# Optimization experiments

Measured on AMD Instinct MI355X. Metric: run time of the kernel, lower is better.

Reference implementation:

```python
import jax, jax.numpy as jnp
import numpy as np

NEG_INF = float('-inf')


def setup_inputs() -> dict:
    key = jax.random.key(0)
    k1, k2, k3, k4 = jax.random.split(key, 4)
    B, S, D, C = 32, 1024, 1024, 64
    emb_sentences = jax.random.normal(k1, (B, S, D), dtype=jnp.float32)
    att_sentences = jax.random.bernoulli(k2, 0.5, (B, S))
    W = jax.random.normal(k3, (D, C), dtype=jnp.float32) * (1.0 / np.sqrt(D))
    b = jax.random.normal(k4, (C,), dtype=jnp.float32) * 0.01
    return {"emb_sentences": emb_sentences, "att_sentences": att_sentences, "W": W, "b": b}


def reference(emb_sentences, att_sentences, W, b):
    # Original: gather valid tokens -> Linear classifier -> scatter into
    # a -inf-filled [B, S, C] logits tensor. Dense-equivalent (jit-friendly):
    # compute logits everywhere and mask invalid positions to -inf; masked
    # tokens never flow through the MLP in the original, and jnp.where
    # reproduces exactly that (values and gradients).
    dense = jnp.einsum('bsd,dc->bsc', emb_sentences, W) + b  # [B,S,C]
    logits = jnp.where(att_sentences[:, :, None], dense, NEG_INF)
    # get_labels: argmax, then -1 wherever the row was -inf-filled
    labels = jnp.argmax(logits, axis=-1)
    labels = jnp.where(logits[:, :, 0] == NEG_INF, -1, labels)
    return labels, logits
```

## Files before the change

kernel.cpp:

```cpp
#include <hip/hip_runtime.h>
#include <hip/hip_bf16.h>
#include <hip/hip_fp16.h>
#include <math.h>
#include <float.h>

#define ROWS 32768
#define DDIM 1024
#define CDIM 64

#define MASKED_LOGIT_BITS 0xFF7F0000u

typedef __attribute__((ext_vector_type(8))) _Float16 f16x8;
typedef __attribute__((ext_vector_type(4))) float f32x4;

#define BFRAG_BYTES (32 * 2 * 4 * 64 * 16)

__device__ __forceinline__ void split8(float4 a, float4 b, f16x8& h, f16x8& l) {
    float f[8] = {a.x, a.y, a.z, a.w, b.x, b.y, b.z, b.w};
#pragma unroll
    for (int j = 0; j < 8; ++j) {
        _Float16 t = (_Float16)f[j];
        h[j] = t;
        l[j] = (_Float16)(f[j] - (float)t);
    }
}

__global__ __launch_bounds__(256) void bprep_kernel(const float* __restrict__ W,
                                                    unsigned char* __restrict__ bf) {
    const int ks = blockIdx.x;
    const int t  = threadIdx.x;
    const int g  = t >> 6, c = t & 63;
    float vv[8];
#pragma unroll
    for (int j = 0; j < 8; ++j)
        vv[j] = W[(size_t)(ks * 32 + g * 8 + j) * CDIM + c];
    f16x8 hi, lo;
    split8(make_float4(vv[0], vv[1], vv[2], vv[3]),
           make_float4(vv[4], vv[5], vv[6], vv[7]), hi, lo);
    const int nt = c >> 4;
    const int lane = g * 16 + (c & 15);
    *(f16x8*)(bf + ((size_t)((ks * 2 + 0) * 4 + nt) * 64 + lane) * 16) = hi;
    *(f16x8*)(bf + ((size_t)((ks * 2 + 1) * 4 + nt) * 64 + lane) * 16) = lo;
}

#define MBR 64
#define NRND 8
#define KSR 128

__global__ __launch_bounds__(512, 4) void dense_mfma_kernel(
    const float* __restrict__ emb, const int* __restrict__ att,
    const unsigned char* __restrict__ bf, const float* __restrict__ bias,
    float* __restrict__ out) {
    __shared__ f16x8 Af[4][2][4][64];
    __shared__ f16x8 Bl[4][2][4][64];
    __shared__ float pv[4][16][2], pc[4][16][2];

    const int start = blockIdx.x * MBR;
    const int tid = threadIdx.x;
    const int lane = tid & 63;
    const int wv = tid >> 6;
    const int mr = wv & 3, np = wv >> 2;

    const int srow = tid & 63;
    const int kseg = (tid >> 6) * 16;
    const bool sval = (att[start + srow] != 0);
    const float* __restrict__ sp = emb + (size_t)(start + srow) * DDIM + kseg;
    const int ssub = kseg >> 5;
    const int sg0  = (kseg & 31) >> 3;
    const int smr  = srow >> 4;
    const int sl0  = sg0 * 16 + (srow & 15);
    const int sl1  = sl0 + 16;

    const f16x8* __restrict__ bsrc0 = (const f16x8*)bf + (size_t)tid * 4;
    f16x8* const bdst = (f16x8*)Bl + (size_t)tid * 4;

    f32x4 hh0 = {0,0,0,0}, ml0 = {0,0,0,0}, hh1 = {0,0,0,0}, ml1 = {0,0,0,0};

    float4 x0 = {0,0,0,0}, x1 = {0,0,0,0}, x2 = {0,0,0,0}, x3 = {0,0,0,0};
    if (sval) {
        x0 = *(const float4*)(sp);
        x1 = *(const float4*)(sp + 4);
        x2 = *(const float4*)(sp + 8);
        x3 = *(const float4*)(sp + 12);
    }
    f16x8 y0 = bsrc0[0], y1 = bsrc0[1], y2 = bsrc0[2], y3 = bsrc0[3];

    const int nt0 = np * 2, nt1 = np * 2 + 1;

#pragma unroll 1
    for (int t = 0; t < NRND; ++t) {
        __syncthreads();
        {
            f16x8 h0, l0, h1, l1;
            split8(x0, x1, h0, l0);
            split8(x2, x3, h1, l1);
            Af[ssub][0][smr][sl0] = h0;
            Af[ssub][1][smr][sl0] = l0;
            Af[ssub][0][smr][sl1] = h1;
            Af[ssub][1][smr][sl1] = l1;
            bdst[0] = y0; bdst[1] = y1; bdst[2] = y2; bdst[3] = y3;
        }
        __syncthreads();

        const bool more = (t + 1 < NRND);
        if (more) {
            if (sval) {
                const float* q = sp + (t + 1) * KSR;
                x0 = *(const float4*)(q);
                x1 = *(const float4*)(q + 4);
                x2 = *(const float4*)(q + 8);
                x3 = *(const float4*)(q + 12);
            }
            const f16x8* bs = bsrc0 + (size_t)(t + 1) * 2048;
            y0 = bs[0]; y1 = bs[1]; y2 = bs[2]; y3 = bs[3];
        }

#pragma unroll
        for (int s = 0; s < 4; ++s) {
            f16x8 ah = Af[s][0][mr][lane];
            f16x8 al = Af[s][1][mr][lane];
            f16x8 bh0 = Bl[s][0][nt0][lane];
            f16x8 bl0 = Bl[s][1][nt0][lane];
            f16x8 bh1 = Bl[s][0][nt1][lane];
            f16x8 bl1 = Bl[s][1][nt1][lane];
            hh0 = __builtin_amdgcn_mfma_f32_16x16x32_f16(ah, bh0, hh0, 0, 0, 0);
            ml0 = __builtin_amdgcn_mfma_f32_16x16x32_f16(al, bh0, ml0, 0, 0, 0);
            ml0 = __builtin_amdgcn_mfma_f32_16x16x32_f16(ah, bl0, ml0, 0, 0, 0);
            hh1 = __builtin_amdgcn_mfma_f32_16x16x32_f16(ah, bh1, hh1, 0, 0, 0);
            ml1 = __builtin_amdgcn_mfma_f32_16x16x32_f16(al, bh1, ml1, 0, 0, 0);
            ml1 = __builtin_amdgcn_mfma_f32_16x16x32_f16(ah, bl1, ml1, 0, 0, 0);
        }
    }

    f32x4 c0 = hh0 + ml0;
    f32x4 c1 = hh1 + ml1;
    const int n0 = np * 32 + (lane & 15);
    const float bz0 = bias[n0], bz1 = bias[n0 + 16];
    const float sent = __uint_as_float(MASKED_LOGIT_BITS);
    float* labels = out;
    float* logits = out + ROWS;

#pragma unroll
    for (int q = 0; q < 4; ++q) {
        int rl = mr * 16 + (lane >> 4) * 4 + q;
        int grow = start + rl;
        bool v = (att[grow] != 0);
        float v0 = v ? (c0[q] + bz0) : sent;
        float v1 = v ? (c1[q] + bz1) : sent;
        logits[(size_t)grow * CDIM + n0]      = v0;
        logits[(size_t)grow * CDIM + n0 + 16] = v1;
        float bv; float bc;
        if (v1 > v0) { bv = v1; bc = (float)(n0 + 16); }
        else         { bv = v0; bc = (float)n0; }
#pragma unroll
        for (int m = 1; m < 16; m <<= 1) {
            float ov = __shfl_xor(bv, m);
            float oc = __shfl_xor(bc, m);
            if (ov > bv || (ov == bv && oc < bc)) { bv = ov; bc = oc; }
        }
        if ((lane & 15) == 0) { pv[mr][rl & 15][np] = bv; pc[mr][rl & 15][np] = bc; }
    }
    __syncthreads();

    if (tid < MBR) {
        int grow = start + tid;
        if (att[grow] != 0) {
            int m = tid >> 4, r = tid & 15;
            labels[grow] = (pv[m][r][1] > pv[m][r][0]) ? pc[m][r][1] : pc[m][r][0];
        } else {
            labels[grow] = -1.0f;
        }
    }
}

#define BR 16
#define KT 64
#define NQ 4
#define NRv 4
#define QSPAN (NRv * KT)

__global__ void zero_counter_kernel(int* __restrict__ cnt) {
    if (threadIdx.x == 0) *cnt = 0;
}

__global__ __launch_bounds__(256) void compact_kernel(const int* __restrict__ att,
                                                      float* __restrict__ out,
                                                      int* __restrict__ cnt,
                                                      int* __restrict__ list) {
    int row = blockIdx.x * 256 + threadIdx.x;
    int lane = threadIdx.x & 63;
    bool valid = (att[row] != 0);
    unsigned long long ball = __ballot(valid);
    int total = __popcll(ball);
    int base = 0;
    if (lane == 0 && total > 0) base = atomicAdd(cnt, total);
    base = __shfl(base, 0);
    if (valid) {
        int prefix = __popcll(ball & ((1ull << lane) - 1ull));
        list[base + prefix] = row;
    } else {
        out[row] = -1.0f;
    }
}

__global__ __launch_bounds__(256) void fill_kernel(const int* __restrict__ att,
                                                   float* __restrict__ out) {
    int gid = blockIdx.x * 256 + threadIdx.x;
    int row = gid >> 4;
    int q   = gid & 15;
    if (att[row] != 0) return;
    float s = __uint_as_float(MASKED_LOGIT_BITS);
    float4 sv = make_float4(s, s, s, s);
    float* logits = out + ROWS;
    *(float4*)(logits + (size_t)row * CDIM + q * 4) = sv;
}

__global__ __launch_bounds__(512, 8) void row_gemm_kernel(const float* __restrict__ emb,
                                                          const float* __restrict__ W,
                                                          const float* __restrict__ bias,
                                                          const int* __restrict__ cnt,
                                                          const int* __restrict__ list,
                                                          float* __restrict__ out) {
    __shared__ float smem[2 * NQ * BR * KT];
    const int nValid = *cnt;
    const int start = blockIdx.x * BR;
    if (start >= nValid) return;
    const int tid  = threadIdx.x;
    const int lane = tid & 63;
    const int wv   = tid >> 6;
    const int q    = wv >> 1;
    const int rg   = (wv & 1) * 8;
    const int srow = tid >> 5;
    const int sq   = (tid >> 3) & 3;
    const int soff = (tid & 7) * 4;
    int sidx = start + srow;
    int sr = list[(sidx < nValid) ? sidx : start];
    const float* __restrict__ sp = emb + (size_t)sr * DDIM + sq * QSPAN + soff;
    float* const sdst0 = &smem[((0 * NQ + sq) * BR + srow) * KT + soff];
    float* const sdst1 = &smem[((1 * NQ + sq) * BR + srow) * KT + soff];
    float acc[8];
#pragma unroll
    for (int r = 0; r < 8; ++r) acc[r] = 0.0f;
    {
        float4 a0 = *(const float4*)(sp);
        float4 a1 = *(const float4*)(sp + 32);
        *(float4*)(sdst0)      = a0;
        *(float4*)(sdst0 + 32) = a1;
    }
    __syncthreads();
    const float* const ebase0 = &smem[((0 * NQ + q) * BR + rg) * KT];
    const float* const ebase1 = &smem[((1 * NQ + q) * BR + rg) * KT];
#pragma unroll 1
    for (int t = 0; t < NRv; ++t) {
        float4 n0, n1;
        const bool more = (t + 1 < NRv);
        if (more) {
            const float* qq = sp + (t + 1) * KT;
            n0 = *(const float4*)(qq);
            n1 = *(const float4*)(qq + 32);
        }
        const float* __restrict__ wp = W + (size_t)(q * QSPAN + t * KT) * CDIM + lane;
        const float* __restrict__ eb = (t & 1) ? ebase1 : ebase0;
#pragma unroll 2
        for (int c8 = 0; c8 < KT; c8 += 8) {
            float w0 = wp[0 * CDIM]; float w1 = wp[1 * CDIM];
            float w2 = wp[2 * CDIM]; float w3 = wp[3 * CDIM];
            float w4 = wp[4 * CDIM]; float w5 = wp[5 * CDIM];
            float w6 = wp[6 * CDIM]; float w7 = wp[7 * CDIM];
            wp += 8 * CDIM;
            const float* ep0 = eb + c8;
#pragma unroll
            for (int r = 0; r < 8; ++r) {
                const float* ep = ep0 + r * KT;
                float4 ea = *(const float4*)(ep);
                float4 ev = *(const float4*)(ep + 4);
                acc[r] = fmaf(ea.x, w0, acc[r]); acc[r] = fmaf(ea.y, w1, acc[r]);
                acc[r] = fmaf(ea.z, w2, acc[r]); acc[r] = fmaf(ea.w, w3, acc[r]);
                acc[r] = fmaf(ev.x, w4, acc[r]); acc[r] = fmaf(ev.y, w5, acc[r]);
                acc[r] = fmaf(ev.z, w6, acc[r]); acc[r] = fmaf(ev.w, w7, acc[r]);
            }
        }
        if (more) {
            float* d = (t & 1) ? sdst0 : sdst1;
            *(float4*)(d)      = n0;
            *(float4*)(d + 32) = n1;
        }
        __syncthreads();
    }
    if (q != 0) {
#pragma unroll
        for (int r = 0; r < 8; ++r)
            smem[((q - 1) * BR + rg + r) * 64 + lane] = acc[r];
    }
    __syncthreads();
    if (q == 0) {
        float* labels = out;
        float* logits = out + ROWS;
        const float bz = bias[lane];
#pragma unroll
        for (int r = 0; r < 8; ++r) {
            int idx = start + rg + r;
            bool v = (idx < nValid);
            int row = list[v ? idx : start];
            float s = acc[r] + bz
                    + smem[((0 * BR) + rg + r) * 64 + lane]
                    + smem[((1 * BR) + rg + r) * 64 + lane]
                    + smem[((2 * BR) + rg + r) * 64 + lane];
            if (v) logits[(size_t)row * CDIM + lane] = s;
            float bv = s; int bc = lane;
#pragma unroll
            for (int m = 1; m < 64; m <<= 1) {
                float ov = __shfl_xor(bv, m);
                int   oc = __shfl_xor(bc, m);
                if (ov > bv || (ov == bv && oc < bc)) { bv = ov; bc = oc; }
            }
            if (lane == 0 && v) labels[row] = (float)bc;
        }
    }
}

extern "C" void kernel_launch(void* const* d_in, const int* in_sizes, int n_in,
                              void* d_out, int out_size, void* d_ws, size_t ws_size,
                              hipStream_t stream) {
    const float* emb  = (const float*)d_in[0];
    const int*   att  = (const int*)d_in[1];
    const float* W    = (const float*)d_in[2];
    const float* bias = (const float*)d_in[3];
    float* out = (float*)d_out;

    if (ws_size >= (size_t)BFRAG_BYTES) {
        unsigned char* bf = (unsigned char*)d_ws;
        bprep_kernel<<<32, 256, 0, stream>>>(W, bf);
        dense_mfma_kernel<<<ROWS / MBR, 512, 0, stream>>>(emb, att, bf, bias, out);
    } else {
        int* cnt  = (int*)d_ws;
        int* list = (int*)d_ws + 64;
        zero_counter_kernel<<<1, 64, 0, stream>>>(cnt);
        compact_kernel<<<ROWS / 256, 256, 0, stream>>>(att, out, cnt, list);
        fill_kernel<<<(ROWS * 16) / 256, 256, 0, stream>>>(att, out);
        row_gemm_kernel<<<ROWS / BR, 512, 0, stream>>>(emb, W, bias, cnt, list, out);
    }
}
```

Measured before the change: 37.92 us.

## Fuse W fp16 split into MFMA kernel and drop prep and fallback kernels

```diff
diff --git a/kernel.cpp b/kernel.cpp
--- a/kernel.cpp
+++ b/kernel.cpp
@@ -13,8 +13,6 @@
 typedef __attribute__((ext_vector_type(8))) _Float16 f16x8;
 typedef __attribute__((ext_vector_type(4))) float f32x4;
 
-#define BFRAG_BYTES (32 * 2 * 4 * 64 * 16)
-
 __device__ __forceinline__ void split8(float4 a, float4 b, f16x8& h, f16x8& l) {
     float f[8] = {a.x, a.y, a.z, a.w, b.x, b.y, b.z, b.w};
 #pragma unroll
@@ -25,31 +23,13 @@
     }
 }
 
-__global__ __launch_bounds__(256) void bprep_kernel(const float* __restrict__ W,
-                                                    unsigned char* __restrict__ bf) {
-    const int ks = blockIdx.x;
-    const int t  = threadIdx.x;
-    const int g  = t >> 6, c = t & 63;
-    float vv[8];
-#pragma unroll
-    for (int j = 0; j < 8; ++j)
-        vv[j] = W[(size_t)(ks * 32 + g * 8 + j) * CDIM + c];
-    f16x8 hi, lo;
-    split8(make_float4(vv[0], vv[1], vv[2], vv[3]),
-           make_float4(vv[4], vv[5], vv[6], vv[7]), hi, lo);
-    const int nt = c >> 4;
-    const int lane = g * 16 + (c & 15);
-    *(f16x8*)(bf + ((size_t)((ks * 2 + 0) * 4 + nt) * 64 + lane) * 16) = hi;
-    *(f16x8*)(bf + ((size_t)((ks * 2 + 1) * 4 + nt) * 64 + lane) * 16) = lo;
-}
-
 #define MBR 64
 #define NRND 8
 #define KSR 128
 
-__global__ __launch_bounds__(512, 4) void dense_mfma_kernel(
+__global__ __launch_bounds__(512, 4) void fused_mfma_kernel(
     const float* __restrict__ emb, const int* __restrict__ att,
-    const unsigned char* __restrict__ bf, const float* __restrict__ bias,
+    const float* __restrict__ W, const float* __restrict__ bias,
     float* __restrict__ out) {
     __shared__ f16x8 Af[4][2][4][64];
     __shared__ f16x8 Bl[4][2][4][64];
@@ -71,8 +51,12 @@
     const int sl0  = sg0 * 16 + (srow & 15);
     const int sl1  = sl0 + 16;
 
-    const f16x8* __restrict__ bsrc0 = (const f16x8*)bf + (size_t)tid * 4;
-    f16x8* const bdst = (f16x8*)Bl + (size_t)tid * 4;
+    const int lf  = tid & 63;
+    const int bnt = (tid >> 6) & 3;
+    const int bs0 = tid >> 8;
+    const int bg  = lf >> 4;
+    const int bn  = bnt * 16 + (lf & 15);
+    const float* __restrict__ wbase = W + bn;
 
     f32x4 hh0 = {0,0,0,0}, ml0 = {0,0,0,0}, hh1 = {0,0,0,0}, ml1 = {0,0,0,0};
 
@@ -83,7 +67,13 @@
         x2 = *(const float4*)(sp + 8);
         x3 = *(const float4*)(sp + 12);
     }
-    f16x8 y0 = bsrc0[0], y1 = bsrc0[1], y2 = bsrc0[2], y3 = bsrc0[3];
+    float wa[8], wb[8];
+#pragma unroll
+    for (int j = 0; j < 8; ++j)
+        wa[j] = wbase[(size_t)(bs0 * 32 + bg * 8 + j) * CDIM];
+#pragma unroll
+    for (int j = 0; j < 8; ++j)
+        wb[j] = wbase[(size_t)((bs0 + 2) * 32 + bg * 8 + j) * CDIM];
 
     const int nt0 = np * 2, nt1 = np * 2 + 1;
 
@@ -98,7 +88,15 @@
             Af[ssub][1][smr][sl0] = l0;
             Af[ssub][0][smr][sl1] = h1;
             Af[ssub][1][smr][sl1] = l1;
-            bdst[0] = y0; bdst[1] = y1; bdst[2] = y2; bdst[3] = y3;
+            f16x8 bh, bl;
+            split8(make_float4(wa[0], wa[1], wa[2], wa[3]),
+                   make_float4(wa[4], wa[5], wa[6], wa[7]), bh, bl);
+            Bl[bs0][0][bnt][lf] = bh;
+            Bl[bs0][1][bnt][lf] = bl;
+            split8(make_float4(wb[0], wb[1], wb[2], wb[3]),
+                   make_float4(wb[4], wb[5], wb[6], wb[7]), bh, bl);
+            Bl[bs0 + 2][0][bnt][lf] = bh;
+            Bl[bs0 + 2][1][bnt][lf] = bl;
         }
         __syncthreads();
 
@@ -111,10 +109,16 @@
                 x2 = *(const float4*)(q + 8);
                 x3 = *(const float4*)(q + 12);
             }
-            const f16x8* bs = bsrc0 + (size_t)(t + 1) * 2048;
-            y0 = bs[0]; y1 = bs[1]; y2 = bs[2]; y3 = bs[3];
+            const float* wk = wbase + (size_t)(t + 1) * KSR * CDIM;
+#pragma unroll
+            for (int j = 0; j < 8; ++j)
+                wa[j] = wk[(size_t)(bs0 * 32 + bg * 8 + j) * CDIM];
+#pragma unroll
+            for (int j = 0; j < 8; ++j)
+                wb[j] = wk[(size_t)((bs0 + 2) * 32 + bg * 8 + j) * CDIM];
         }
 
+        __builtin_amdgcn_s_setprio(1);
 #pragma unroll
         for (int s = 0; s < 4; ++s) {
             f16x8 ah = Af[s][0][mr][lane];
@@ -130,6 +134,7 @@
             ml1 = __builtin_amdgcn_mfma_f32_16x16x32_f16(al, bh1, ml1, 0, 0, 0);
             ml1 = __builtin_amdgcn_mfma_f32_16x16x32_f16(ah, bl1, ml1, 0, 0, 0);
         }
+        __builtin_amdgcn_s_setprio(0);
     }
 
     f32x4 c0 = hh0 + ml0;
@@ -173,152 +178,6 @@
     }
 }
 
-#define BR 16
-#define KT 64
-#define NQ 4
-#define NRv 4
-#define QSPAN (NRv * KT)
-
-__global__ void zero_counter_kernel(int* __restrict__ cnt) {
-    if (threadIdx.x == 0) *cnt = 0;
-}
-
-__global__ __launch_bounds__(256) void compact_kernel(const int* __restrict__ att,
-                                                      float* __restrict__ out,
-                                                      int* __restrict__ cnt,
-                                                      int* __restrict__ list) {
-    int row = blockIdx.x * 256 + threadIdx.x;
-    int lane = threadIdx.x & 63;
-    bool valid = (att[row] != 0);
-    unsigned long long ball = __ballot(valid);
-    int total = __popcll(ball);
-    int base = 0;
-    if (lane == 0 && total > 0) base = atomicAdd(cnt, total);
-    base = __shfl(base, 0);
-    if (valid) {
-        int prefix = __popcll(ball & ((1ull << lane) - 1ull));
-        list[base + prefix] = row;
-    } else {
-        out[row] = -1.0f;
-    }
-}
-
-__global__ __launch_bounds__(256) void fill_kernel(const int* __restrict__ att,
-                                                   float* __restrict__ out) {
-    int gid = blockIdx.x * 256 + threadIdx.x;
-    int row = gid >> 4;
-    int q   = gid & 15;
-    if (att[row] != 0) return;
-    float s = __uint_as_float(MASKED_LOGIT_BITS);
-    float4 sv = make_float4(s, s, s, s);
-    float* logits = out + ROWS;
-    *(float4*)(logits + (size_t)row * CDIM + q * 4) = sv;
-}
-
-__global__ __launch_bounds__(512, 8) void row_gemm_kernel(const float* __restrict__ emb,
-                                                          const float* __restrict__ W,
-                                                          const float* __restrict__ bias,
-                                                          const int* __restrict__ cnt,
-                                                          const int* __restrict__ list,
-                                                          float* __restrict__ out) {
-    __shared__ float smem[2 * NQ * BR * KT];
-    const int nValid = *cnt;
-    const int start = blockIdx.x * BR;
-    if (start >= nValid) return;
-    const int tid  = threadIdx.x;
-    const int lane = tid & 63;
-    const int wv   = tid >> 6;
-    const int q    = wv >> 1;
-    const int rg   = (wv & 1) * 8;
-    const int srow = tid >> 5;
-    const int sq   = (tid >> 3) & 3;
-    const int soff = (tid & 7) * 4;
-    int sidx = start + srow;
-    int sr = list[(sidx < nValid) ? sidx : start];
-    const float* __restrict__ sp = emb + (size_t)sr * DDIM + sq * QSPAN + soff;
-    float* const sdst0 = &smem[((0 * NQ + sq) * BR + srow) * KT + soff];
-    float* const sdst1 = &smem[((1 * NQ + sq) * BR + srow) * KT + soff];
-    float acc[8];
-#pragma unroll
-    for (int r = 0; r < 8; ++r) acc[r] = 0.0f;
-    {
-        float4 a0 = *(const float4*)(sp);
-        float4 a1 = *(const float4*)(sp + 32);
-        *(float4*)(sdst0)      = a0;
-        *(float4*)(sdst0 + 32) = a1;
-    }
-    __syncthreads();
-    const float* const ebase0 = &smem[((0 * NQ + q) * BR + rg) * KT];
-    const float* const ebase1 = &smem[((1 * NQ + q) * BR + rg) * KT];
-#pragma unroll 1
-    for (int t = 0; t < NRv; ++t) {
-        float4 n0, n1;
-        const bool more = (t + 1 < NRv);
-        if (more) {
-            const float* qq = sp + (t + 1) * KT;
-            n0 = *(const float4*)(qq);
-            n1 = *(const float4*)(qq + 32);
-        }
-        const float* __restrict__ wp = W + (size_t)(q * QSPAN + t * KT) * CDIM + lane;
-        const float* __restrict__ eb = (t & 1) ? ebase1 : ebase0;
-#pragma unroll 2
-        for (int c8 = 0; c8 < KT; c8 += 8) {
-            float w0 = wp[0 * CDIM]; float w1 = wp[1 * CDIM];
-            float w2 = wp[2 * CDIM]; float w3 = wp[3 * CDIM];
-            float w4 = wp[4 * CDIM]; float w5 = wp[5 * CDIM];
-            float w6 = wp[6 * CDIM]; float w7 = wp[7 * CDIM];
-            wp += 8 * CDIM;
-            const float* ep0 = eb + c8;
-#pragma unroll
-            for (int r = 0; r < 8; ++r) {
-                const float* ep = ep0 + r * KT;
-                float4 ea = *(const float4*)(ep);
-                float4 ev = *(const float4*)(ep + 4);
-                acc[r] = fmaf(ea.x, w0, acc[r]); acc[r] = fmaf(ea.y, w1, acc[r]);
-                acc[r] = fmaf(ea.z, w2, acc[r]); acc[r] = fmaf(ea.w, w3, acc[r]);
-                acc[r] = fmaf(ev.x, w4, acc[r]); acc[r] = fmaf(ev.y, w5, acc[r]);
-                acc[r] = fmaf(ev.z, w6, acc[r]); acc[r] = fmaf(ev.w, w7, acc[r]);
-            }
-        }
-        if (more) {
-            float* d = (t & 1) ? sdst0 : sdst1;
-            *(float4*)(d)      = n0;
-            *(float4*)(d + 32) = n1;
-        }
-        __syncthreads();
-    }
-    if (q != 0) {
-#pragma unroll
-        for (int r = 0; r < 8; ++r)
-            smem[((q - 1) * BR + rg + r) * 64 + lane] = acc[r];
-    }
-    __syncthreads();
-    if (q == 0) {
-        float* labels = out;
-        float* logits = out + ROWS;
-        const float bz = bias[lane];
-#pragma unroll
-        for (int r = 0; r < 8; ++r) {
-            int idx = start + rg + r;
-            bool v = (idx < nValid);
-            int row = list[v ? idx : start];
-            float s = acc[r] + bz
-                    + smem[((0 * BR) + rg + r) * 64 + lane]
-                    + smem[((1 * BR) + rg + r) * 64 + lane]
-                    + smem[((2 * BR) + rg + r) * 64 + lane];
-            if (v) logits[(size_t)row * CDIM + lane] = s;
-            float bv = s; int bc = lane;
-#pragma unroll
-            for (int m = 1; m < 64; m <<= 1) {
-                float ov = __shfl_xor(bv, m);
-                int   oc = __shfl_xor(bc, m);
-                if (ov > bv || (ov == bv && oc < bc)) { bv = ov; bc = oc; }
-            }
-            if (lane == 0 && v) labels[row] = (float)bc;
-        }
-    }
-}
-
 extern "C" void kernel_launch(void* const* d_in, const int* in_sizes, int n_in,
                               void* d_out, int out_size, void* d_ws, size_t ws_size,
                               hipStream_t stream) {
@@ -328,16 +187,6 @@
     const float* bias = (const float*)d_in[3];
     float* out = (float*)d_out;
 
-    if (ws_size >= (size_t)BFRAG_BYTES) {
-        unsigned char* bf = (unsigned char*)d_ws;
-        bprep_kernel<<<32, 256, 0, stream>>>(W, bf);
-        dense_mfma_kernel<<<ROWS / MBR, 512, 0, stream>>>(emb, att, bf, bias, out);
-    } else {
-        int* cnt  = (int*)d_ws;
-        int* list = (int*)d_ws + 64;
-        zero_counter_kernel<<<1, 64, 0, stream>>>(cnt);
-        compact_kernel<<<ROWS / 256, 256, 0, stream>>>(att, out, cnt, list);
-        fill_kernel<<<(ROWS * 16) / 256, 256, 0, stream>>>(att, out);
-        row_gemm_kernel<<<ROWS / BR, 512, 0, stream>>>(emb, W, bias, cnt, list, out);
-    }
+    (void)d_ws; (void)ws_size;
+    fused_mfma_kernel<<<ROWS / MBR, 512, 0, stream>>>(emb, att, W, bias, out);
 }
```

New measurement: 31.42 us (median of 2 runs). 1.21x faster.
